# Optimization experiments

Hardware: AMD Instinct MI355X
Metric: run time of the kernel (lower is better)

Reference implementation:

```python
import jax, jax.numpy as jnp
import numpy as np
from jax import lax

D_MODEL = 512
D_STATE = 16
D_CONV = 4
DT_RANK = 32  # ceil(512/16)


def setup_inputs() -> dict:
    key = jax.random.key(0)
    ks = jax.random.split(key, 8)
    B, L = 4, 2048
    x = jax.random.normal(ks[0], (B, L, D_MODEL), dtype=jnp.float32)
    A_log = jax.random.normal(ks[1], (D_MODEL, D_STATE), dtype=jnp.float32)
    D = jax.random.normal(ks[2], (D_MODEL,), dtype=jnp.float32)
    # torch Linear weight layout: (out_features, in_features)
    x_proj_w = jax.random.normal(ks[3], (DT_RANK + 2 * D_STATE, D_MODEL), dtype=jnp.float32) * (1.0 / np.sqrt(D_MODEL))
    dt_proj_w = jax.random.normal(ks[4], (D_MODEL, DT_RANK), dtype=jnp.float32) * (1.0 / np.sqrt(DT_RANK))
    dt_proj_b = jax.random.normal(ks[5], (D_MODEL,), dtype=jnp.float32) * 0.1
    # depthwise conv: (out_channels, in_channels/groups=1, kernel)
    conv_w = jax.random.normal(ks[6], (D_MODEL, 1, D_CONV), dtype=jnp.float32) * (1.0 / np.sqrt(D_CONV))
    conv_b = jax.random.normal(ks[7], (D_MODEL,), dtype=jnp.float32) * 0.1
    return {"x": x, "A_log": A_log, "D": D, "x_proj_w": x_proj_w,
            "dt_proj_w": dt_proj_w, "dt_proj_b": dt_proj_b,
            "conv_w": conv_w, "conv_b": conv_b}


def reference(x, A_log, D, x_proj_w, dt_proj_w, dt_proj_b, conv_w, conv_b):
    B, L, d_model = x.shape
    # causal depthwise conv1d: torch pads (d_conv-1) both sides then trims right -> left-pad only
    x_t = jnp.transpose(x, (0, 2, 1))  # (B, d, L)
    xc = lax.conv_general_dilated(
        x_t, conv_w, window_strides=(1,), padding=[(D_CONV - 1, 0)],
        feature_group_count=d_model)
    xc = xc + conv_b[None, :, None]
    xc = jnp.transpose(xc, (0, 2, 1))  # (B, L, d)

    x_dbl = xc @ x_proj_w.T  # (B, L, dt_rank + 2*d_state)
    dt = x_dbl[..., :DT_RANK]
    Bm = x_dbl[..., DT_RANK:DT_RANK + D_STATE]       # (B, L, n)
    C = x_dbl[..., DT_RANK + D_STATE:]               # (B, L, n)

    dt = jax.nn.softplus(dt @ dt_proj_w.T + dt_proj_b)  # (B, L, d)
    A = -jnp.exp(A_log.astype(jnp.float32))             # (d, n)
    dA = jnp.exp(jnp.einsum('bld,dn->bldn', dt, A))     # (B, L, d, n)
    dBx = jnp.einsum('bld,bln->bldn', dt * xc, Bm)      # (B, L, d, n)

    def step(h, inputs):
        dA_t, dBx_t, C_t = inputs  # (B,d,n), (B,d,n), (B,n)
        h = dA_t * h + dBx_t
        y_t = jnp.einsum('bdn,bn->bd', h, C_t)
        return h, y_t

    h0 = jnp.zeros((B, d_model, D_STATE), dtype=x.dtype)
    _, ys = lax.scan(step, h0, (jnp.moveaxis(dA, 1, 0), jnp.moveaxis(dBx, 1, 0), jnp.moveaxis(C, 1, 0)))
    y = jnp.moveaxis(ys, 0, 1)  # (B, L, d)
    return y + xc * D[None, None, :]
```

## Files before the change

kernel.cpp:

```cpp
#include <hip/hip_runtime.h>
#include <stdint.h>

#define L_SEQ   2048
#define NBATCH  4
#define DM      512
#define DS      16
#define DR      32
#define NROWS   8192
#define NBDN    32768
#define NCH     64
#define CL      32
#define LOG2E   1.4426950408889634f

#define WS_DX    0
#define WS_XDBL  4194304
#define WS_WXT   4718592
#define WS_WDTT  4751360
#define WS_A2    4767744
#define WS_DTSUM 4775936
#define WS_S     4907008

__device__ __forceinline__ uint32_t bf16_rne_hi(float v) {
    uint32_t u = __float_as_uint(v);
    u += 0x7FFF + ((u >> 16) & 1);
    return u & 0xFFFF0000u;
}

__global__ void k_prep(const float* __restrict__ Wx, const float* __restrict__ Wdt,
                       const float* __restrict__ A_log,
                       float* __restrict__ WxT, float* __restrict__ WdtT,
                       float* __restrict__ A2) {
    int idx = blockIdx.x * 256 + threadIdx.x;
    if (idx < DM * 64) {
        int d = idx >> 6, j = idx & 63;
        WxT[idx] = Wx[j * DM + d];
    }
    if (idx < DR * DM) {
        int r = idx >> 9, d = idx & 511;
        WdtT[idx] = Wdt[d * DR + r];
    }
    if (idx < DM * DS)
        A2[idx] = -__expf(A_log[idx]) * LOG2E;
}

__global__ void __launch_bounds__(256) k_front(
        const float* __restrict__ x, const float* __restrict__ convw,
        const float* __restrict__ convb, const float* __restrict__ WxT,
        const float* __restrict__ WdtT, const float* __restrict__ dtb,
        uint32_t* __restrict__ dx, float* __restrict__ xdbl) {
    __shared__ float xcs[8][512];
    __shared__ float pt[4][8][64];
    __shared__ float xds[8][64];
    int t  = threadIdx.x;
    int r0 = blockIdx.x * 8;
    int b  = r0 >> 11, l0 = r0 & (L_SEQ - 1);
    int dq = t & 127, half = t >> 7;

    {
        const float4* wp = (const float4*)convw;
        float4 w0 = wp[dq * 4 + 0], w1 = wp[dq * 4 + 1];
        float4 w2 = wp[dq * 4 + 2], w3 = wp[dq * 4 + 3];
        float4 bias = ((const float4*)convb)[dq];
        #pragma unroll
        for (int i = 0; i < 4; ++i) {
            int row = half * 4 + i;
            int l   = l0 + row;
            const float* xr = x + ((size_t)(b * L_SEQ + l)) * DM + dq * 4;
            float4 acc = bias;
            float4 xv = *(const float4*)xr;
            acc.x = fmaf(xv.x, w0.w, acc.x); acc.y = fmaf(xv.y, w1.w, acc.y);
            acc.z = fmaf(xv.z, w2.w, acc.z); acc.w = fmaf(xv.w, w3.w, acc.w);
            if (l >= 1) {
                xv = *(const float4*)(xr - DM);
                acc.x = fmaf(xv.x, w0.z, acc.x); acc.y = fmaf(xv.y, w1.z, acc.y);
                acc.z = fmaf(xv.z, w2.z, acc.z); acc.w = fmaf(xv.w, w3.z, acc.w);
            }
            if (l >= 2) {
                xv = *(const float4*)(xr - 2 * DM);
                acc.x = fmaf(xv.x, w0.y, acc.x); acc.y = fmaf(xv.y, w1.y, acc.y);
                acc.z = fmaf(xv.z, w2.y, acc.z); acc.w = fmaf(xv.w, w3.y, acc.w);
            }
            if (l >= 3) {
                xv = *(const float4*)(xr - 3 * DM);
                acc.x = fmaf(xv.x, w0.x, acc.x); acc.y = fmaf(xv.y, w1.x, acc.y);
                acc.z = fmaf(xv.z, w2.x, acc.z); acc.w = fmaf(xv.w, w3.x, acc.w);
            }
            *(float4*)(&xcs[row][dq * 4]) = acc;
        }
    }
    __syncthreads();

    {
        int wv = t >> 6, j = t & 63;
        int k0 = wv * 128;
        float acc[8] = {0.f, 0.f, 0.f, 0.f, 0.f, 0.f, 0.f, 0.f};
        const float* wp = WxT + (size_t)k0 * 64 + j;
        for (int k4 = 0; k4 < 32; ++k4) {
            float4 xr[8];
            #pragma unroll
            for (int ri = 0; ri < 8; ++ri)
                xr[ri] = *(const float4*)(&xcs[ri][k0 + k4 * 4]);
            #pragma unroll
            for (int kk = 0; kk < 4; ++kk) {
                float w = wp[(k4 * 4 + kk) * 64];
                acc[0] = fmaf(((const float*)&xr[0])[kk], w, acc[0]);
                acc[1] = fmaf(((const float*)&xr[1])[kk], w, acc[1]);
                acc[2] = fmaf(((const float*)&xr[2])[kk], w, acc[2]);
                acc[3] = fmaf(((const float*)&xr[3])[kk], w, acc[3]);
                acc[4] = fmaf(((const float*)&xr[4])[kk], w, acc[4]);
                acc[5] = fmaf(((const float*)&xr[5])[kk], w, acc[5]);
                acc[6] = fmaf(((const float*)&xr[6])[kk], w, acc[6]);
                acc[7] = fmaf(((const float*)&xr[7])[kk], w, acc[7]);
            }
        }
        #pragma unroll
        for (int ri = 0; ri < 8; ++ri) pt[wv][ri][j] = acc[ri];
    }
    __syncthreads();

    #pragma unroll
    for (int o = t; o < 512; o += 256) {
        int row = o >> 6, j2 = o & 63;
        float s = (pt[0][row][j2] + pt[1][row][j2])
                + (pt[2][row][j2] + pt[3][row][j2]);
        xds[row][j2] = s;
        xdbl[(size_t)(r0 + row) * 64 + j2] = s;
    }
    __syncthreads();

    {
        float4 bias = ((const float4*)dtb)[dq];
        float4 z0 = bias, z1 = bias, z2 = bias, z3 = bias;
        for (int r = 0; r < DR; ++r) {
            float4 w4 = *(const float4*)(WdtT + r * DM + dq * 4);
            float x0 = xds[half * 4 + 0][r];
            float x1 = xds[half * 4 + 1][r];
            float x2 = xds[half * 4 + 2][r];
            float x3 = xds[half * 4 + 3][r];
            z0.x = fmaf(x0, w4.x, z0.x); z0.y = fmaf(x0, w4.y, z0.y);
            z0.z = fmaf(x0, w4.z, z0.z); z0.w = fmaf(x0, w4.w, z0.w);
            z1.x = fmaf(x1, w4.x, z1.x); z1.y = fmaf(x1, w4.y, z1.y);
            z1.z = fmaf(x1, w4.z, z1.z); z1.w = fmaf(x1, w4.w, z1.w);
            z2.x = fmaf(x2, w4.x, z2.x); z2.y = fmaf(x2, w4.y, z2.y);
            z2.z = fmaf(x2, w4.z, z2.z); z2.w = fmaf(x2, w4.w, z2.w);
            z3.x = fmaf(x3, w4.x, z3.x); z3.y = fmaf(x3, w4.y, z3.y);
            z3.z = fmaf(x3, w4.z, z3.z); z3.w = fmaf(x3, w4.w, z3.w);
        }
        float4 zz[4] = {z0, z1, z2, z3};
        #pragma unroll
        for (int i = 0; i < 4; ++i) {
            int row = half * 4 + i;
            float4 zi = zz[i];
            float4 sp;
            sp.x = fmaxf(zi.x, 0.f) + log1pf(__expf(-fabsf(zi.x)));
            sp.y = fmaxf(zi.y, 0.f) + log1pf(__expf(-fabsf(zi.y)));
            sp.z = fmaxf(zi.z, 0.f) + log1pf(__expf(-fabsf(zi.z)));
            sp.w = fmaxf(zi.w, 0.f) + log1pf(__expf(-fabsf(zi.w)));
            uint4 pk;
            pk.x = bf16_rne_hi(sp.x) | (bf16_rne_hi(xcs[row][dq * 4 + 0]) >> 16);
            pk.y = bf16_rne_hi(sp.y) | (bf16_rne_hi(xcs[row][dq * 4 + 1]) >> 16);
            pk.z = bf16_rne_hi(sp.z) | (bf16_rne_hi(xcs[row][dq * 4 + 2]) >> 16);
            pk.w = bf16_rne_hi(sp.w) | (bf16_rne_hi(xcs[row][dq * 4 + 3]) >> 16);
            *(uint4*)(dx + ((size_t)(b * L_SEQ + l0 + row)) * DM + dq * 4) = pk;
        }
    }
}

__global__ void __launch_bounds__(256) k_scan1(
        const uint32_t* __restrict__ dx, const float* __restrict__ xdbl,
        const float* __restrict__ A2, float* __restrict__ S,
        float* __restrict__ dtsum) {
    int lane   = threadIdx.x & 63;
    int wv     = threadIdx.x >> 6;
    int dlocal = lane & 15;
    int nq     = lane >> 4;
    int db8    = blockIdx.x & 7;
    int c      = blockIdx.x >> 3;
    int b      = blockIdx.y;
    int d      = (db8 * 4 + wv) * 16 + dlocal;

    float4 a2 = *(const float4*)(A2 + (size_t)d * DS + nq * 4);
    float h0 = 0.f, h1 = 0.f, h2 = 0.f, h3 = 0.f;
    float dsum = 0.f;

    int l0 = c * CL;
    const uint32_t* dxp = dx + ((size_t)(b * L_SEQ + l0)) * DM + d;
    const float*    bp  = xdbl + ((size_t)(b * L_SEQ + l0)) * 64 + DR + nq * 4;

    #pragma unroll 4
    for (int i = 0; i < CL; ++i) {
        uint32_t v = dxp[(size_t)i * DM];
        float dt = __uint_as_float(v & 0xFFFF0000u);
        float xv = __uint_as_float(v << 16);
        float4 B4 = *(const float4*)(bp + (size_t)i * 64);
        float u = dt * xv;
        dsum += dt;
        float dA;
        dA = exp2f(dt * a2.x); h0 = fmaf(dA, h0, u * B4.x);
        dA = exp2f(dt * a2.y); h1 = fmaf(dA, h1, u * B4.y);
        dA = exp2f(dt * a2.z); h2 = fmaf(dA, h2, u * B4.z);
        dA = exp2f(dt * a2.w); h3 = fmaf(dA, h3, u * B4.w);
    }

    float4 sv; sv.x = h0; sv.y = h1; sv.z = h2; sv.w = h3;
    *(float4*)(S + (size_t)c * NBDN + ((size_t)(b * DM + d)) * DS + nq * 4) = sv;
    if (nq == 0)
        dtsum[c * (NBATCH * DM) + b * DM + d] = dsum;
}

__global__ void k_scan2(const float* __restrict__ dtsum, const float* __restrict__ A2,
                        float* __restrict__ S) {
    int t  = blockIdx.x * 256 + threadIdx.x;
    float a2 = A2[t & (DM * DS - 1)];
    int bd = t >> 4;
    float H = 0.f;
    #pragma unroll 8
    for (int c = 0; c < NCH; ++c) {
        float p = exp2f(a2 * dtsum[c * (NBATCH * DM) + bd]);
        float s = S[(size_t)c * NBDN + t];
        S[(size_t)c * NBDN + t] = H;
        H = fmaf(p, H, s);
    }
}

__global__ void __launch_bounds__(256) k_scan3(
        const uint32_t* __restrict__ dx, const float* __restrict__ xdbl,
        const float* __restrict__ A2, const float* __restrict__ Dvec,
        const float* __restrict__ Hin, float* __restrict__ out) {
    int lane   = threadIdx.x & 63;
    int wv     = threadIdx.x >> 6;
    int dlocal = lane & 15;
    int nq     = lane >> 4;
    int db8    = blockIdx.x & 7;
    int c      = blockIdx.x >> 3;
    int b      = blockIdx.y;
    int d      = (db8 * 4 + wv) * 16 + dlocal;

    float4 a2 = *(const float4*)(A2 + (size_t)d * DS + nq * 4);
    float Dv = Dvec[d];
    float4 hv = *(const float4*)(Hin + (size_t)c * NBDN + ((size_t)(b * DM + d)) * DS + nq * 4);
    float h0 = hv.x, h1 = hv.y, h2 = hv.z, h3 = hv.w;

    int l0 = c * CL;
    const uint32_t* dxp = dx + ((size_t)(b * L_SEQ + l0)) * DM + d;
    const float*    bp  = xdbl + ((size_t)(b * L_SEQ + l0)) * 64 + DR + nq * 4;
    float* op = out + ((size_t)(b * L_SEQ + l0)) * DM + d;

    #pragma unroll 4
    for (int i = 0; i < CL; ++i) {
        uint32_t v = dxp[(size_t)i * DM];
        float dt = __uint_as_float(v & 0xFFFF0000u);
        float xv = __uint_as_float(v << 16);
        float4 B4 = *(const float4*)(bp + (size_t)i * 64);
        float4 C4 = *(const float4*)(bp + (size_t)i * 64 + DS);
        float u = dt * xv;
        float dA;
        dA = exp2f(dt * a2.x); h0 = fmaf(dA, h0, u * B4.x);
        dA = exp2f(dt * a2.y); h1 = fmaf(dA, h1, u * B4.y);
        dA = exp2f(dt * a2.z); h2 = fmaf(dA, h2, u * B4.z);
        dA = exp2f(dt * a2.w); h3 = fmaf(dA, h3, u * B4.w);
        float p = fmaf(h3, C4.w, fmaf(h2, C4.z, fmaf(h1, C4.y, h0 * C4.x)));
        p += __shfl_xor(p, 16);
        p += __shfl_xor(p, 32);
        if (nq == 0) op[(size_t)i * DM] = fmaf(xv, Dv, p);
    }
}

extern "C" void kernel_launch(void* const* d_in, const int* in_sizes, int n_in,
                              void* d_out, int out_size, void* d_ws, size_t ws_size,
                              hipStream_t stream) {
    const float* x      = (const float*)d_in[0];
    const float* A_log  = (const float*)d_in[1];
    const float* Dvec   = (const float*)d_in[2];
    const float* Wx     = (const float*)d_in[3];
    const float* Wdt    = (const float*)d_in[4];
    const float* dtb    = (const float*)d_in[5];
    const float* convw  = (const float*)d_in[6];
    const float* convb  = (const float*)d_in[7];
    float* out = (float*)d_out;
    float* ws  = (float*)d_ws;

    uint32_t* dxp = (uint32_t*)(ws + WS_DX);
    float* xdbl  = ws + WS_XDBL;
    float* WxT   = ws + WS_WXT;
    float* WdtT  = ws + WS_WDTT;
    float* A2    = ws + WS_A2;
    float* dtsum = ws + WS_DTSUM;
    float* S     = ws + WS_S;

    k_prep<<<128, 256, 0, stream>>>(Wx, Wdt, A_log, WxT, WdtT, A2);
    k_front<<<1024, 256, 0, stream>>>(x, convw, convb, WxT, WdtT, dtb, dxp, xdbl);
    k_scan1<<<dim3(8 * NCH, NBATCH), 256, 0, stream>>>(dxp, xdbl, A2, S, dtsum);
    k_scan2<<<128, 256, 0, stream>>>(dtsum, A2, S);
    k_scan3<<<dim3(8 * NCH, NBATCH), 256, 0, stream>>>(dxp, xdbl, A2, Dvec, S, out);
}
```

Measured before the change: 94.57 us.

## Fuse chunk-carry scan into output scan and halve chunk count

```diff
diff --git a/kernel.cpp b/kernel.cpp
--- a/kernel.cpp
+++ b/kernel.cpp
@@ -6,10 +6,9 @@
 #define DM      512
 #define DS      16
 #define DR      32
-#define NROWS   8192
 #define NBDN    32768
-#define NCH     64
-#define CL      32
+#define NCH     32
+#define CL      64
 #define LOG2E   1.4426950408889634f
 
 #define WS_DX    0
@@ -18,7 +17,7 @@
 #define WS_WDTT  4751360
 #define WS_A2    4767744
 #define WS_DTSUM 4775936
-#define WS_S     4907008
+#define WS_S     4841472
 
 __device__ __forceinline__ uint32_t bf16_rne_hi(float v) {
     uint32_t u = __float_as_uint(v);
@@ -26,18 +25,18 @@
     return u & 0xFFFF0000u;
 }
 
-__global__ void k_prep(const float* __restrict__ Wx, const float* __restrict__ Wdt,
-                       const float* __restrict__ A_log,
-                       float* __restrict__ WxT, float* __restrict__ WdtT,
-                       float* __restrict__ A2) {
+__global__ void __launch_bounds__(256) k_prep(
+        const float* __restrict__ Wx, const float* __restrict__ Wdt,
+        const float* __restrict__ A_log, float* __restrict__ WxT,
+        float* __restrict__ WdtT, float* __restrict__ A2) {
     int idx = blockIdx.x * 256 + threadIdx.x;
     if (idx < DM * 64) {
-        int d = idx >> 6, j = idx & 63;
-        WxT[idx] = Wx[j * DM + d];
+        int dd = idx >> 6, j = idx & 63;
+        WxT[idx] = Wx[j * DM + dd];
     }
     if (idx < DR * DM) {
-        int r = idx >> 9, d = idx & 511;
-        WdtT[idx] = Wdt[d * DR + r];
+        int r = idx >> 9, dd = idx & 511;
+        WdtT[idx] = Wdt[dd * DR + r];
     }
     if (idx < DM * DS)
         A2[idx] = -__expf(A_log[idx]) * LOG2E;
@@ -170,95 +169,96 @@
         const uint32_t* __restrict__ dx, const float* __restrict__ xdbl,
         const float* __restrict__ A2, float* __restrict__ S,
         float* __restrict__ dtsum) {
-    int lane   = threadIdx.x & 63;
-    int wv     = threadIdx.x >> 6;
+    int t      = threadIdx.x;
+    int u      = blockIdx.x;
+    int lane   = t & 63;
+    int wv     = t >> 6;
     int dlocal = lane & 15;
     int nq     = lane >> 4;
-    int db8    = blockIdx.x & 7;
-    int c      = blockIdx.x >> 3;
-    int b      = blockIdx.y;
+    int db8    = u & 7;
+    int c      = (u >> 3) & (NCH - 1);
+    int b      = u >> 8;
     int d      = (db8 * 4 + wv) * 16 + dlocal;
+    int l0     = c * CL;
 
     float4 a2 = *(const float4*)(A2 + (size_t)d * DS + nq * 4);
     float h0 = 0.f, h1 = 0.f, h2 = 0.f, h3 = 0.f;
     float dsum = 0.f;
-
-    int l0 = c * CL;
     const uint32_t* dxp = dx + ((size_t)(b * L_SEQ + l0)) * DM + d;
     const float*    bp  = xdbl + ((size_t)(b * L_SEQ + l0)) * 64 + DR + nq * 4;
 
-    #pragma unroll 4
+    #pragma unroll 8
     for (int i = 0; i < CL; ++i) {
         uint32_t v = dxp[(size_t)i * DM];
         float dt = __uint_as_float(v & 0xFFFF0000u);
         float xv = __uint_as_float(v << 16);
         float4 B4 = *(const float4*)(bp + (size_t)i * 64);
-        float u = dt * xv;
+        float uu = dt * xv;
         dsum += dt;
         float dA;
-        dA = exp2f(dt * a2.x); h0 = fmaf(dA, h0, u * B4.x);
-        dA = exp2f(dt * a2.y); h1 = fmaf(dA, h1, u * B4.y);
-        dA = exp2f(dt * a2.z); h2 = fmaf(dA, h2, u * B4.z);
-        dA = exp2f(dt * a2.w); h3 = fmaf(dA, h3, u * B4.w);
-    }
-
+        dA = exp2f(dt * a2.x); h0 = fmaf(dA, h0, uu * B4.x);
+        dA = exp2f(dt * a2.y); h1 = fmaf(dA, h1, uu * B4.y);
+        dA = exp2f(dt * a2.z); h2 = fmaf(dA, h2, uu * B4.z);
+        dA = exp2f(dt * a2.w); h3 = fmaf(dA, h3, uu * B4.w);
+    }
     float4 sv; sv.x = h0; sv.y = h1; sv.z = h2; sv.w = h3;
     *(float4*)(S + (size_t)c * NBDN + ((size_t)(b * DM + d)) * DS + nq * 4) = sv;
     if (nq == 0)
         dtsum[c * (NBATCH * DM) + b * DM + d] = dsum;
 }
 
-__global__ void k_scan2(const float* __restrict__ dtsum, const float* __restrict__ A2,
-                        float* __restrict__ S) {
-    int t  = blockIdx.x * 256 + threadIdx.x;
-    float a2 = A2[t & (DM * DS - 1)];
-    int bd = t >> 4;
-    float H = 0.f;
-    #pragma unroll 8
-    for (int c = 0; c < NCH; ++c) {
-        float p = exp2f(a2 * dtsum[c * (NBATCH * DM) + bd]);
-        float s = S[(size_t)c * NBDN + t];
-        S[(size_t)c * NBDN + t] = H;
-        H = fmaf(p, H, s);
-    }
-}
-
-__global__ void __launch_bounds__(256) k_scan3(
+__global__ void __launch_bounds__(256) k_scan23(
         const uint32_t* __restrict__ dx, const float* __restrict__ xdbl,
         const float* __restrict__ A2, const float* __restrict__ Dvec,
-        const float* __restrict__ Hin, float* __restrict__ out) {
-    int lane   = threadIdx.x & 63;
-    int wv     = threadIdx.x >> 6;
+        const float* __restrict__ S, const float* __restrict__ dtsum,
+        float* __restrict__ out) {
+    int t      = threadIdx.x;
+    int u      = blockIdx.x;
+    int lane   = t & 63;
+    int wv     = t >> 6;
     int dlocal = lane & 15;
     int nq     = lane >> 4;
-    int db8    = blockIdx.x & 7;
-    int c      = blockIdx.x >> 3;
-    int b      = blockIdx.y;
+    int db8    = u & 7;
+    int c      = (u >> 3) & (NCH - 1);
+    int b      = u >> 8;
     int d      = (db8 * 4 + wv) * 16 + dlocal;
+    int l0     = c * CL;
 
     float4 a2 = *(const float4*)(A2 + (size_t)d * DS + nq * 4);
-    float Dv = Dvec[d];
-    float4 hv = *(const float4*)(Hin + (size_t)c * NBDN + ((size_t)(b * DM + d)) * DS + nq * 4);
-    float h0 = hv.x, h1 = hv.y, h2 = hv.z, h3 = hv.w;
-
-    int l0 = c * CL;
+    float Dv  = Dvec[d];
+
+    float h0 = 0.f, h1 = 0.f, h2 = 0.f, h3 = 0.f;
+    {
+        const float* dsp = dtsum + b * DM + d;
+        const float* Sp  = S + ((size_t)(b * DM + d)) * DS + nq * 4;
+        for (int cc = 0; cc < c; ++cc) {
+            float ds  = dsp[cc * (NBATCH * DM)];
+            float4 Sc = *(const float4*)(Sp + (size_t)cc * NBDN);
+            float p;
+            p = exp2f(a2.x * ds); h0 = fmaf(p, h0, Sc.x);
+            p = exp2f(a2.y * ds); h1 = fmaf(p, h1, Sc.y);
+            p = exp2f(a2.z * ds); h2 = fmaf(p, h2, Sc.z);
+            p = exp2f(a2.w * ds); h3 = fmaf(p, h3, Sc.w);
+        }
+    }
+
     const uint32_t* dxp = dx + ((size_t)(b * L_SEQ + l0)) * DM + d;
     const float*    bp  = xdbl + ((size_t)(b * L_SEQ + l0)) * 64 + DR + nq * 4;
     float* op = out + ((size_t)(b * L_SEQ + l0)) * DM + d;
 
-    #pragma unroll 4
+    #pragma unroll 8
     for (int i = 0; i < CL; ++i) {
         uint32_t v = dxp[(size_t)i * DM];
         float dt = __uint_as_float(v & 0xFFFF0000u);
         float xv = __uint_as_float(v << 16);
         float4 B4 = *(const float4*)(bp + (size_t)i * 64);
         float4 C4 = *(const float4*)(bp + (size_t)i * 64 + DS);
-        float u = dt * xv;
+        float uu = dt * xv;
         float dA;
-        dA = exp2f(dt * a2.x); h0 = fmaf(dA, h0, u * B4.x);
-        dA = exp2f(dt * a2.y); h1 = fmaf(dA, h1, u * B4.y);
-        dA = exp2f(dt * a2.z); h2 = fmaf(dA, h2, u * B4.z);
-        dA = exp2f(dt * a2.w); h3 = fmaf(dA, h3, u * B4.w);
+        dA = exp2f(dt * a2.x); h0 = fmaf(dA, h0, uu * B4.x);
+        dA = exp2f(dt * a2.y); h1 = fmaf(dA, h1, uu * B4.y);
+        dA = exp2f(dt * a2.z); h2 = fmaf(dA, h2, uu * B4.z);
+        dA = exp2f(dt * a2.w); h3 = fmaf(dA, h3, uu * B4.w);
         float p = fmaf(h3, C4.w, fmaf(h2, C4.z, fmaf(h1, C4.y, h0 * C4.x)));
         p += __shfl_xor(p, 16);
         p += __shfl_xor(p, 32);
@@ -278,19 +278,18 @@
     const float* convw  = (const float*)d_in[6];
     const float* convb  = (const float*)d_in[7];
     float* out = (float*)d_out;
-    float* ws  = (float*)d_ws;
-
-    uint32_t* dxp = (uint32_t*)(ws + WS_DX);
-    float* xdbl  = ws + WS_XDBL;
-    float* WxT   = ws + WS_WXT;
-    float* WdtT  = ws + WS_WDTT;
-    float* A2    = ws + WS_A2;
-    float* dtsum = ws + WS_DTSUM;
-    float* S     = ws + WS_S;
+    float* wsf = (float*)d_ws;
+
+    uint32_t* dx    = (uint32_t*)(wsf + WS_DX);
+    float*    xdbl  = wsf + WS_XDBL;
+    float*    WxT   = wsf + WS_WXT;
+    float*    WdtT  = wsf + WS_WDTT;
+    float*    A2    = wsf + WS_A2;
+    float*    dtsum = wsf + WS_DTSUM;
+    float*    S     = wsf + WS_S;
 
     k_prep<<<128, 256, 0, stream>>>(Wx, Wdt, A_log, WxT, WdtT, A2);
-    k_front<<<1024, 256, 0, stream>>>(x, convw, convb, WxT, WdtT, dtb, dxp, xdbl);
-    k_scan1<<<dim3(8 * NCH, NBATCH), 256, 0, stream>>>(dxp, xdbl, A2, S, dtsum);
-    k_scan2<<<128, 256, 0, stream>>>(dtsum, A2, S);
-    k_scan3<<<dim3(8 * NCH, NBATCH), 256, 0, stream>>>(dxp, xdbl, A2, Dvec, S, out);
-}
+    k_front<<<1024, 256, 0, stream>>>(x, convw, convb, WxT, WdtT, dtb, dx, xdbl);
+    k_scan1<<<1024, 256, 0, stream>>>(dx, xdbl, A2, S, dtsum);
+    k_scan23<<<1024, 256, 0, stream>>>(dx, xdbl, A2, Dvec, S, dtsum, out);
+}
```

Result: slower. 131.0 us (+38.5%).
